# Optimization experiments

Measured on AMD Instinct MI355X. Metric: run time of the kernel, lower is better.

Reference implementation:

```python
import jax, jax.numpy as jnp
import numpy as np

B, C, H, W = 4, 256, 128, 128
HEADS = 64
HD = C // HEADS  # 4
G = 32           # group norm groups
EPS = 1e-5


def setup_inputs() -> dict:
    key = jax.random.key(0)
    ks = jax.random.split(key, 6)
    x = jax.random.normal(ks[0], (B, C, H, W), dtype=jnp.float32)
    gn_weight = jnp.ones((1, C, 1, 1), dtype=jnp.float32)
    gn_bias = jnp.zeros((1, C, 1, 1), dtype=jnp.float32)
    # 1x1 convs stored as (out_ch, in_ch) matrices
    qkv_w = jax.random.normal(ks[1], (3 * C, C), dtype=jnp.float32) * 0.02
    qkv_b = jax.random.normal(ks[2], (3 * C,), dtype=jnp.float32) * 0.01
    out_w = jax.random.normal(ks[3], (C, C), dtype=jnp.float32) * 0.02
    out_b = jax.random.normal(ks[4], (C,), dtype=jnp.float32) * 0.01
    return {"x": x, "gn_weight": gn_weight, "gn_bias": gn_bias,
            "qkv_w": qkv_w, "qkv_b": qkv_b, "out_w": out_w, "out_b": out_b}


def group_norm(x, weight, bias):
    n, c, h, w = x.shape
    xg = x.reshape(n, G, -1)
    mean = xg.mean(axis=-1, keepdims=True)
    var = jnp.var(xg, axis=-1, keepdims=True, ddof=1)  # torch.var default is unbiased
    xg = (xg - mean) / jnp.sqrt(var + EPS)
    return xg.reshape(n, c, h, w) * weight + bias


def conv1x1(x, w, b):
    # x: (B, Cin, H, W), w: (Cout, Cin)
    return jnp.einsum('bchw,oc->bohw', x, w) + b[None, :, None, None]


def reference(x, gn_weight, gn_bias, qkv_w, qkv_b, out_w, out_b):
    skip = x
    h = group_norm(x, gn_weight, gn_bias)
    qkv = conv1x1(h, qkv_w, qkv_b)                      # (B, 3C, H, W)
    qkv = qkv.reshape(B, HEADS, 3 * HD, H * W)
    q, k, v = jnp.split(qkv, 3, axis=2)                  # each (B, heads, hd, HW)
    scores = jnp.einsum('bhdn,bhen->bhde', q, k) / (HD ** 0.5)  # (B, heads, hd, hd)
    scores = jax.nn.softmax(scores, axis=1)              # softmax over HEADS axis (as in source)
    out = jnp.einsum('bhde,bhen->bhdn', scores, v)       # (B, heads, hd, HW)
    out = out.reshape(B, C, H, W)
    out = conv1x1(out, out_w, out_b)
    return out + skip
```

## Files before the change

kernel.cpp:

```cpp
#include <hip/hip_runtime.h>


constexpr int kB = 4;
constexpr int kC = 256;
constexpr int kHW = 16384;
constexpr int kHeads = 64;
constexpr int kNG = 32;
constexpr int kCPG = 8;
constexpr int kCP1 = 257;
constexpr int kPS = 260;
constexpr float kEPS = 1e-5f;
constexpr int kNSplit = 32;

typedef __attribute__((ext_vector_type(8))) _Float16 f16x8;
typedef __attribute__((ext_vector_type(4))) _Float16 f16x4;
typedef __attribute__((ext_vector_type(4))) float f32x4;

union V8 { f16x8 v; uint4 u; _Float16 h[8]; };

__device__ __forceinline__ void gload16(const void* g, void* l) {
  __builtin_amdgcn_global_load_lds(
      (const __attribute__((address_space(1))) void*)g,
      (__attribute__((address_space(3))) void*)l, 16, 0, 0);
}

constexpr size_t oXT    = 0;
constexpr size_t oXH    = oXT + (size_t)kB * kHW * kC / 2;
constexpr size_t oSpart = oXH + (size_t)kB * kHW * kC / 2;
constexpr size_t oS     = oSpart + (size_t)3 * kB * kNSplit * 128 * 128;
constexpr size_t oSums  = oS + (size_t)kB * kCP1 * kPS;
constexpr size_t oGv    = oSums + (size_t)kB * kC;
constexpr size_t oSc    = oGv + (size_t)kB * kC;
constexpr size_t oTc    = oSc + (size_t)kB * kC;
constexpr size_t oScore = oTc + (size_t)kB * kC;
constexpr size_t oAq    = oSpart;
constexpr size_t oM     = oXH;
constexpr size_t oGmH   = oXH + (size_t)kB * kC * kPS;

__global__ __launch_bounds__(256) void k0_tr(const float* __restrict__ x,
                                             _Float16* __restrict__ xT,
                                             _Float16* __restrict__ xH,
                                             float* __restrict__ sums) {
  const int nt = blockIdx.x, ct = blockIdx.y, b = blockIdx.z;
  __shared__ float T[64][65];
  __shared__ float psum[64][4];
  const float* xb = x + ((size_t)b * kC + ct * 64) * kHW + nt * 64;
  _Float16* xhb = xH + ((size_t)b * kC + ct * 64) * kHW + nt * 64;
  const int tid = threadIdx.x;

#pragma unroll
  for (int rep = 0; rep < 4; ++rep) {
    const int r = rep * 16 + (tid >> 4);
    const int c4 = (tid & 15) * 4;
    float4 v = *(const float4*)(xb + (size_t)r * kHW + c4);
    T[r][c4 + 0] = v.x; T[r][c4 + 1] = v.y; T[r][c4 + 2] = v.z; T[r][c4 + 3] = v.w;
    f16x4 hv = {(_Float16)v.x, (_Float16)v.y, (_Float16)v.z, (_Float16)v.w};
    *(f16x4*)(xhb + (size_t)r * kHW + c4) = hv;
  }
  __syncthreads();
  {
    const int q = tid >> 6, r = tid & 63;
    float s = 0.f;
#pragma unroll
    for (int i = 0; i < 16; ++i) s += T[r][q * 16 + i];
    psum[r][q] = s;
  }
  __syncthreads();
  if (tid < 64) {
    float s = psum[tid][0] + psum[tid][1] + psum[tid][2] + psum[tid][3];
    atomicAdd(&sums[b * kC + ct * 64 + tid], s);
  }
  const int nl = tid >> 2, cgrp = tid & 3;
  V8 lo, hi;
#pragma unroll
  for (int i = 0; i < 8; ++i)  lo.h[i] = (_Float16)T[cgrp * 16 + i][nl];
#pragma unroll
  for (int i = 0; i < 8; ++i)  hi.h[i] = (_Float16)T[cgrp * 16 + 8 + i][nl];
  _Float16* dst = xT + ((size_t)b * kHW + nt * 64 + nl) * kC + ct * 64 + cgrp * 16;
  *(uint4*)dst = lo.u;
  *(uint4*)(dst + 8) = hi.u;
}

__global__ __launch_bounds__(256) void k1_syrk(const _Float16* __restrict__ xH,
                                               float* __restrict__ Spart) {
  const int tt = blockIdx.x >> 5;
  const int sp = blockIdx.x & 31;
  const int b = blockIdx.y;
  const int ti = (tt == 2) ? 1 : 0;
  const int tj = (tt == 0) ? 0 : 1;
  const bool diag = (ti == tj);
  const _Float16* xb = xH + (size_t)b * kC * kHW;
  const int n0 = sp * (kHW / kNSplit);

  __shared__ __align__(16) _Float16 XI[2][128 * 64];
  __shared__ __align__(16) _Float16 XJ[2][128 * 64];

  const int tid = threadIdx.x;
  const int wave = tid >> 6, lane = tid & 63;
  const int wi = wave >> 1, wj = wave & 1;
  const int lrow = lane & 15, lgq = lane >> 4;
  const int srow = lane >> 3, sslot = lane & 7;

  const _Float16* srcI = xb + (size_t)(ti * 128) * kHW + n0;
  const _Float16* srcJ = xb + (size_t)(tj * 128) * kHW + n0;

  f32x4 acc[16];
#pragma unroll
  for (int i = 0; i < 16; ++i) acc[i] = (f32x4){0.f, 0.f, 0.f, 0.f};

  auto stage = [&](int buf, int nb) {
#pragma unroll
    for (int rep = 0; rep < 4; ++rep) {
      const int rr = rep * 32 + wave * 8 + srow;
      const int g = sslot ^ (rr & 7);
      char* dI = (char*)XI[buf] + (rep * 32 + wave * 8) * 128;
      gload16(srcI + (size_t)rr * kHW + nb + g * 8, dI);
      if (!diag) {
        char* dJ = (char*)XJ[buf] + (rep * 32 + wave * 8) * 128;
        gload16(srcJ + (size_t)rr * kHW + nb + g * 8, dJ);
      }
    }
  };

  stage(0, 0);
  __syncthreads();

  constexpr int NCH = kHW / kNSplit / 64;
  for (int ch = 0; ch < NCH; ++ch) {
    const int buf = ch & 1;
    if (ch + 1 < NCH) stage(buf ^ 1, (ch + 1) * 64);
    const _Float16* XIb = XI[buf];
    const _Float16* XBb = diag ? XI[buf] : XJ[buf];
#pragma unroll
    for (int sub = 0; sub < 2; ++sub) {
      const int gq = sub * 4 + lgq;
      f16x8 afr[4], bfr[4];
#pragma unroll
      for (int ia = 0; ia < 4; ++ia) {
        const int r = wi * 64 + ia * 16 + lrow;
        afr[ia] = *(const f16x8*)((const char*)XIb + (size_t)r * 128 + (((unsigned)(gq ^ (r & 7))) << 4));
      }
#pragma unroll
      for (int jb = 0; jb < 4; ++jb) {
        const int r = wj * 64 + jb * 16 + lrow;
        bfr[jb] = *(const f16x8*)((const char*)XBb + (size_t)r * 128 + (((unsigned)(gq ^ (r & 7))) << 4));
      }
#pragma unroll
      for (int ia = 0; ia < 4; ++ia)
#pragma unroll
        for (int jb = 0; jb < 4; ++jb)
          acc[ia * 4 + jb] = __builtin_amdgcn_mfma_f32_16x16x32_f16(afr[ia], bfr[jb], acc[ia * 4 + jb], 0, 0, 0);
    }
    __syncthreads();
  }
  float* P = Spart + (((size_t)tt * kB + b) * kNSplit + sp) * 16384;
#pragma unroll
  for (int ia = 0; ia < 4; ++ia)
#pragma unroll
    for (int jb = 0; jb < 4; ++jb)
#pragma unroll
      for (int reg = 0; reg < 4; ++reg) {
        const int i = wi * 64 + ia * 16 + lgq * 4 + reg;
        const int j = wj * 64 + jb * 16 + lrow;
        P[(size_t)i * 128 + j] = acc[ia * 4 + jb][reg];
      }
}

__global__ __launch_bounds__(256) void k1r_reduce(const float* __restrict__ Spart,
                                                  float* __restrict__ S) {
  const int blk = blockIdx.x;
  const int tile12 = blk >> 4;
  const int part = blk & 15;
  const int tt = tile12 >> 2, b = tile12 & 3;
  const int rti = (tt == 2) ? 1 : 0;
  const int rtj = (tt == 0) ? 0 : 1;
  const int e0 = part * 1024 + threadIdx.x * 4;
  float4 s = {0.f, 0.f, 0.f, 0.f};
  const float* base = Spart + ((size_t)tt * kB + b) * kNSplit * 16384 + e0;
  for (int sp = 0; sp < kNSplit; ++sp) {
    float4 v = *(const float4*)(base + (size_t)sp * 16384);
    s.x += v.x; s.y += v.y; s.z += v.z; s.w += v.w;
  }
  const int i = e0 >> 7, j = e0 & 127;
  float* Sb = S + (size_t)b * kCP1 * kPS;
  float* dst = Sb + (size_t)(rti * 128 + i) * kPS + rtj * 128 + j;
  dst[0] = s.x; dst[1] = s.y; dst[2] = s.z; dst[3] = s.w;
  if (tt == 1) {
    Sb[(size_t)(128 + j + 0) * kPS + i] = s.x;
    Sb[(size_t)(128 + j + 1) * kPS + i] = s.y;
    Sb[(size_t)(128 + j + 2) * kPS + i] = s.z;
    Sb[(size_t)(128 + j + 3) * kPS + i] = s.w;
  }
}

__global__ __launch_bounds__(256) void k2a_stats(const float* __restrict__ S,
                                                 const float* __restrict__ sums,
                                                 const float* __restrict__ gw,
                                                 const float* __restrict__ gb,
                                                 float* __restrict__ sArr,
                                                 float* __restrict__ tArr) {
  const int b = blockIdx.x;
  const float* Sb = S + (size_t)b * kCP1 * kPS;
  __shared__ float sx[kC], sdg[kC], meanv[kNG], invv[kNG];
  const int c = threadIdx.x;
  sx[c]  = sums[b * kC + c];
  sdg[c] = Sb[(size_t)c * kPS + c];
  __syncthreads();
  if (c < kNG) {
    float sum = 0.f, ssq = 0.f;
    for (int k = 0; k < kCPG; ++k) { sum += sx[c * kCPG + k]; ssq += sdg[c * kCPG + k]; }
    const float n = (float)(kCPG * kHW);
    const float mean = sum / n;
    const float var = (ssq - n * mean * mean) / (n - 1.0f);
    meanv[c] = mean;
    invv[c] = rsqrtf(var + kEPS);
  }
  __syncthreads();
  const int g = c / kCPG;
  const float s = gw[c] * invv[g];
  sArr[b * kC + c] = s;
  tArr[b * kC + c] = gb[c] - meanv[g] * s;
}

__global__ __launch_bounds__(256) void k3a_aq(const float* __restrict__ S,
                                              const float* __restrict__ sums,
                                              const float* __restrict__ sArr,
                                              const float* __restrict__ tArr,
                                              const float* __restrict__ qkv_w,
                                              const float* __restrict__ qkv_b,
                                              float* __restrict__ Aq) {
  const int ct = blockIdx.x, mt = blockIdx.y, b = blockIdx.z;
  const float* Sb = S + (size_t)b * kCP1 * kPS;
  const float HWf = (float)kHW;
  __shared__ float Wt[32][68];
  __shared__ float Gs[32][68];
  __shared__ float shs[kC], sht[kC], shx[kC], shr[kC];
  const int tid = threadIdx.x;
  {
    const float sv = sArr[b * kC + tid];
    const float tv = tArr[b * kC + tid];
    const float xv = sums[b * kC + tid];
    shs[tid] = sv; sht[tid] = tv; shx[tid] = xv;
    shr[tid] = sv * xv + tv * HWf;
  }
  __syncthreads();
  float acc[16];
#pragma unroll
  for (int i = 0; i < 16; ++i) acc[i] = 0.f;
  const int i0 = (tid & 15) * 4;
  const int j0 = (tid >> 4) * 4;
  const int cp0 = ct * 64;

  for (int cb = 0; cb < kC; cb += 32) {
    int idx = tid;
#pragma unroll
    for (int r = 0; r < 2; ++r) {
      const int m = idx >> 3;
      const int c4 = (idx & 7) * 4;
      const int mg = mt * 64 + m;
      const int row = 12 * (mg >> 2) + (mg & 3);
      float4 v = *(const float4*)(qkv_w + (size_t)row * kC + cb + c4);
      Wt[c4 + 0][m] = v.x; Wt[c4 + 1][m] = v.y; Wt[c4 + 2][m] = v.z; Wt[c4 + 3][m] = v.w;
      idx += 256;
    }
    idx = tid;
#pragma unroll
    for (int r = 0; r < 2; ++r) {
      const int cc = idx >> 4;
      const int n4 = (idx & 15) * 4;
      const int rr = cb + cc;
      const float s_r = shs[rr], t_r = sht[rr], x_r = shx[rr];
      float4 o;
      if (cp0 + n4 < kC) {
        float4 v = *(const float4*)(Sb + (size_t)rr * kPS + cp0 + n4);
        const int cp = cp0 + n4;
        o.x = s_r * (shs[cp + 0] * v.x + sht[cp + 0] * x_r) + t_r * shr[cp + 0];
        o.y = s_r * (shs[cp + 1] * v.y + sht[cp + 1] * x_r) + t_r * shr[cp + 1];
        o.z = s_r * (shs[cp + 2] * v.z + sht[cp + 2] * x_r) + t_r * shr[cp + 2];
        o.w = s_r * (shs[cp + 3] * v.w + sht[cp + 3] * x_r) + t_r * shr[cp + 3];
      } else if (cp0 + n4 == kC) {
        o = (float4){s_r * x_r + t_r * HWf, 0.f, 0.f, 0.f};
      } else {
        o = (float4){0.f, 0.f, 0.f, 0.f};
      }
      *(float4*)&Gs[cc][n4] = o;
      idx += 256;
    }
    __syncthreads();
#pragma unroll
    for (int kk = 0; kk < 32; ++kk) {
      float4 a = *(const float4*)&Wt[kk][i0];
      float4 g = *(const float4*)&Gs[kk][j0];
      acc[0]  += a.x * g.x; acc[1]  += a.x * g.y; acc[2]  += a.x * g.z; acc[3]  += a.x * g.w;
      acc[4]  += a.y * g.x; acc[5]  += a.y * g.y; acc[6]  += a.y * g.z; acc[7]  += a.y * g.w;
      acc[8]  += a.z * g.x; acc[9]  += a.z * g.y; acc[10] += a.z * g.z; acc[11] += a.z * g.w;
      acc[12] += a.w * g.x; acc[13] += a.w * g.y; acc[14] += a.w * g.z; acc[15] += a.w * g.w;
    }
    __syncthreads();
  }
#pragma unroll
  for (int mi = 0; mi < 4; ++mi) {
    const int mg = mt * 64 + i0 + mi;
    const float bias = qkv_b[12 * (mg >> 2) + (mg & 3)];
#pragma unroll
    for (int cj = 0; cj < 4; ++cj) {
      const int cp = cp0 + j0 + cj;
      if (cp < kCP1) {
        const float g256 = (cp < kC) ? shr[cp] : HWf;
        Aq[((size_t)b * kC + mg) * kCP1 + cp] = acc[mi * 4 + cj] + bias * g256;
      }
    }
  }
}

__global__ __launch_bounds__(256) void k3b_scores(const float* __restrict__ Aq,
                                                  const float* __restrict__ qkv_w,
                                                  const float* __restrict__ qkv_b,
                                                  float* __restrict__ score) {
  const int h = blockIdx.x, b = blockIdx.y;
  const int tid = threadIdx.x, wave = tid >> 6, lane = tid & 63;
#pragma unroll
  for (int p = wave; p < 16; p += 4) {
    const int d = p >> 2, e = p & 3;
    const float* aqr = Aq + ((size_t)b * kC + h * 4 + d) * kCP1;
    const int krow = h * 12 + 4 + e;
    float s = 0.f;
#pragma unroll
    for (int it = 0; it < 4; ++it) {
      const int cp = lane + it * 64;
      s += aqr[cp] * qkv_w[(size_t)krow * kC + cp];
    }
    if (lane == 0) s += aqr[256] * qkv_b[krow];
#pragma unroll
    for (int off = 32; off; off >>= 1) s += __shfl_xor(s, off);
    if (lane == 0) score[((size_t)(b * kHeads) + h) * 16 + p] = 0.5f * s;
  }
}

__global__ __launch_bounds__(256) void k45_M(const float* __restrict__ score,
                                             const float* __restrict__ qkv_w,
                                             const float* __restrict__ qkv_b,
                                             float* __restrict__ M) {
  const int b = blockIdx.y;
  const int cidx = blockIdx.x;
  const int h = cidx >> 2, d = cidx & 3;
  __shared__ float sc[64][4];
  __shared__ float mx[4], sm[4];
  const int tid = threadIdx.x;
  {
    const int h2 = tid >> 2, e = tid & 3;
    sc[h2][e] = score[((size_t)(b * kHeads) + h2) * 16 + d * 4 + e];
  }
  __syncthreads();
  const int wave = tid >> 6, lane = tid & 63;
  {
    const float v = sc[lane][wave];
    float m = v;
#pragma unroll
    for (int off = 32; off; off >>= 1) m = fmaxf(m, __shfl_xor(m, off));
    float e2 = expf(v - m);
#pragma unroll
    for (int off = 32; off; off >>= 1) e2 += __shfl_xor(e2, off);
    if (lane == 0) { mx[wave] = m; sm[wave] = e2; }
  }
  __syncthreads();
  const float p0 = expf(sc[h][0] - mx[0]) / sm[0];
  const float p1 = expf(sc[h][1] - mx[1]) / sm[1];
  const float p2 = expf(sc[h][2] - mx[2]) / sm[2];
  const float p3 = expf(sc[h][3] - mx[3]) / sm[3];
  for (int cp = tid; cp < kCP1; cp += 256) {
    float a;
    if (cp < kC) {
      a = p0 * qkv_w[(size_t)(h * 12 + 8 + 0) * kC + cp] +
          p1 * qkv_w[(size_t)(h * 12 + 8 + 1) * kC + cp] +
          p2 * qkv_w[(size_t)(h * 12 + 8 + 2) * kC + cp] +
          p3 * qkv_w[(size_t)(h * 12 + 8 + 3) * kC + cp];
    } else {
      a = p0 * qkv_b[h * 12 + 8 + 0] + p1 * qkv_b[h * 12 + 8 + 1] +
          p2 * qkv_b[h * 12 + 8 + 2] + p3 * qkv_b[h * 12 + 8 + 3];
    }
    M[((size_t)b * kC + cidx) * kPS + cp] = a;
  }
}

__global__ __launch_bounds__(256) void k5b_gemm(const float* __restrict__ M,
                                                const float* __restrict__ out_w,
                                                const float* __restrict__ sArr,
                                                const float* __restrict__ tArr,
                                                _Float16* __restrict__ GmH,
                                                float* __restrict__ gvec) {
  const int ct = blockIdx.x, ot = blockIdx.y, b = blockIdx.z;
  const float* Mb = M + (size_t)b * kC * kPS;
  __shared__ float Wt[32][68];
  __shared__ float Gs[32][68];
  __shared__ float gred[64][17];
  float acc[16];
#pragma unroll
  for (int i = 0; i < 16; ++i) acc[i] = 0.f;
  const int tid = threadIdx.x;
  const int i0 = (tid & 15) * 4;
  const int j0 = (tid >> 4) * 4;
  const int cp0 = ct * 64;

  for (int cb = 0; cb < kC; cb += 32) {
    int idx = tid;
#pragma unroll
    for (int r = 0; r < 2; ++r) {
      const int m = idx >> 3;
      const int c4 = (idx & 7) * 4;
      float4 v = *(const float4*)(out_w + (size_t)(ot * 64 + m) * kC + cb + c4);
      Wt[c4 + 0][m] = v.x; Wt[c4 + 1][m] = v.y; Wt[c4 + 2][m] = v.z; Wt[c4 + 3][m] = v.w;
      idx += 256;
    }
    idx = tid;
#pragma unroll
    for (int r = 0; r < 2; ++r) {
      const int cc = idx >> 4;
      const int n4 = (idx & 15) * 4;
      float4 v = {0.f, 0.f, 0.f, 0.f};
      if (cp0 + n4 < kCP1) v = *(const float4*)(Mb + (size_t)(cb + cc) * kPS + cp0 + n4);
      *(float4*)&Gs[cc][n4] = v;
      idx += 256;
    }
    __syncthreads();
#pragma unroll
    for (int kk = 0; kk < 32; ++kk) {
      float4 a = *(const float4*)&Wt[kk][i0];
      float4 g = *(const float4*)&Gs[kk][j0];
      acc[0]  += a.x * g.x; acc[1]  += a.x * g.y; acc[2]  += a.x * g.z; acc[3]  += a.x * g.w;
      acc[4]  += a.y * g.x; acc[5]  += a.y * g.y; acc[6]  += a.y * g.z; acc[7]  += a.y * g.w;
      acc[8]  += a.z * g.x; acc[9]  += a.z * g.y; acc[10] += a.z * g.z; acc[11] += a.z * g.w;
      acc[12] += a.w * g.x; acc[13] += a.w * g.y; acc[14] += a.w * g.z; acc[15] += a.w * g.w;
    }
    __syncthreads();
  }
  float gpart[4] = {0.f, 0.f, 0.f, 0.f};
#pragma unroll
  for (int mi = 0; mi < 4; ++mi) {
    const int o = ot * 64 + i0 + mi;
#pragma unroll
    for (int cj = 0; cj < 4; ++cj) {
      const int cp = cp0 + j0 + cj;
      const float f = acc[mi * 4 + cj];
      if (cp < kC) {
        GmH[((size_t)b * kC + o) * kC + cp] = (_Float16)(f * sArr[b * kC + cp]);
        gpart[mi] += f * tArr[b * kC + cp];
      } else if (cp == kC) {
        gpart[mi] += f;
      }
    }
  }
#pragma unroll
  for (int mi = 0; mi < 4; ++mi) gred[i0 + mi][tid >> 4] = gpart[mi];
  __syncthreads();
  if (tid < 64) {
    float s = 0.f;
#pragma unroll
    for (int k = 0; k < 16; ++k) s += gred[tid][k];
    atomicAdd(&gvec[b * kC + ot * 64 + tid], s);
  }
}

__global__ __launch_bounds__(256) void k6_final(const _Float16* __restrict__ xT,
                                                const _Float16* __restrict__ GmH,
                                                const float* __restrict__ gvec,
                                                const float* __restrict__ out_b,
                                                const float* __restrict__ x,
                                                float* __restrict__ out) {
  const int nt = blockIdx.x, ot = blockIdx.y, b = blockIdx.z;
  __shared__ __align__(16) char smem[64 * 132 * 4];
  float* Ep = (float*)smem;
  const int tid = threadIdx.x;
  const int wave = tid >> 6, lane = tid & 63;
  const int wo = wave >> 1, wn = wave & 1;
  const int lrow = lane & 15, lgq = lane >> 4;
  const int srow = lane >> 3, sslot = lane & 7;

  const _Float16* xrow = xT + ((size_t)b * kHW + nt * 128) * kC;
  const _Float16* Grow = GmH + (size_t)(b * kC + ot * 128) * kC;

  auto stage = [&](int buf, int cc) {
#pragma unroll
    for (int rep = 0; rep < 4; ++rep) {
      const int rr = rep * 32 + wave * 8 + srow;
      const int g = sslot ^ (rr & 7);
      gload16(xrow + (size_t)rr * kC + cc + g * 8,
              smem + buf * 16384 + (rep * 32 + wave * 8) * 128);
    }
  };

  f32x4 acc[16];
#pragma unroll
  for (int i = 0; i < 16; ++i) acc[i] = (f32x4){0.f, 0.f, 0.f, 0.f};

  stage(0, 0);
  __syncthreads();

  for (int ci = 0; ci < 4; ++ci) {
    const int cc = ci * 64;
    const int buf = ci & 1;
    if (ci < 3) stage(buf ^ 1, cc + 64);
    const char* XB = smem + buf * 16384;
#pragma unroll
    for (int sub = 0; sub < 2; ++sub) {
      const int gq = sub * 4 + lgq;
      f16x8 afr[4], bfr[4];
#pragma unroll
      for (int ia = 0; ia < 4; ++ia) {
        const int r = wo * 64 + ia * 16 + lrow;
        afr[ia] = *(const f16x8*)(Grow + (size_t)r * kC + cc + gq * 8);
      }
#pragma unroll
      for (int jb = 0; jb < 4; ++jb) {
        const int r = wn * 64 + jb * 16 + lrow;
        bfr[jb] = *(const f16x8*)(XB + (size_t)r * 128 + (((unsigned)(gq ^ (r & 7))) << 4));
      }
#pragma unroll
      for (int ia = 0; ia < 4; ++ia)
#pragma unroll
        for (int jb = 0; jb < 4; ++jb)
          acc[ia * 4 + jb] = __builtin_amdgcn_mfma_f32_16x16x32_f16(afr[ia], bfr[jb], acc[ia * 4 + jb], 0, 0, 0);
    }
    __syncthreads();
  }
#pragma unroll
  for (int p = 0; p < 2; ++p) {
    if (wo == p) {
#pragma unroll
      for (int ia = 0; ia < 4; ++ia)
#pragma unroll
        for (int jb = 0; jb < 4; ++jb)
#pragma unroll
          for (int reg = 0; reg < 4; ++reg)
            Ep[(size_t)(ia * 16 + lgq * 4 + reg) * 132 + wn * 64 + jb * 16 + lrow] =
                acc[ia * 4 + jb][reg];
    }
    __syncthreads();
#pragma unroll
    for (int it = 0; it < 8; ++it) {
      const int id = it * 256 + tid;
      const int row = id >> 5, nc = (id & 31) * 4;
      const int o = ot * 128 + p * 64 + row;
      const float gvv = gvec[b * kC + o] + out_b[o];
      float4 e = *(const float4*)&Ep[(size_t)row * 132 + nc];
      const size_t gidx = ((size_t)b * kC + o) * kHW + nt * 128 + nc;
      float4 sk = *(const float4*)&x[gidx];
      float4 res = {e.x + gvv + sk.x, e.y + gvv + sk.y, e.z + gvv + sk.z, e.w + gvv + sk.w};
      *(float4*)&out[gidx] = res;
    }
    __syncthreads();
  }
}

extern "C" void kernel_launch(void* const* d_in, const int* in_sizes, int n_in,
                              void* d_out, int out_size, void* d_ws, size_t ws_size,
                              hipStream_t stream) {
  const float* x    = (const float*)d_in[0];
  const float* gnw  = (const float*)d_in[1];
  const float* gnb  = (const float*)d_in[2];
  const float* qkvw = (const float*)d_in[3];
  const float* qkvb = (const float*)d_in[4];
  const float* outw = (const float*)d_in[5];
  const float* outb = (const float*)d_in[6];
  float* out = (float*)d_out;
  float* ws = (float*)d_ws;

  _Float16* xT   = (_Float16*)(ws + oXT);
  _Float16* xH   = (_Float16*)(ws + oXH);
  float* Spart   = ws + oSpart;
  float* S       = ws + oS;
  float* sums    = ws + oSums;
  float* gv      = ws + oGv;
  float* sArr    = ws + oSc;
  float* tArr    = ws + oTc;
  float* score   = ws + oScore;
  float* Aq      = ws + oAq;
  float* M       = ws + oM;
  _Float16* GmH  = (_Float16*)(ws + oGmH);

  hipMemsetAsync(sums, 0, (size_t)2 * kB * kC * sizeof(float), stream);
  k0_tr<<<dim3(kHW / 64, kC / 64, kB), 256, 0, stream>>>(x, xT, xH, sums);
  k1_syrk<<<dim3(3 * kNSplit, kB), 256, 0, stream>>>(xH, Spart);
  k1r_reduce<<<dim3(3 * kB * 16), 256, 0, stream>>>(Spart, S);
  k2a_stats<<<kB, 256, 0, stream>>>(S, sums, gnw, gnb, sArr, tArr);
  k3a_aq<<<dim3(5, 4, kB), 256, 0, stream>>>(S, sums, sArr, tArr, qkvw, qkvb, Aq);
  k3b_scores<<<dim3(kHeads, kB), 256, 0, stream>>>(Aq, qkvw, qkvb, score);
  k45_M<<<dim3(kC, kB), 256, 0, stream>>>(score, qkvw, qkvb, M);
  k5b_gemm<<<dim3(5, 4, kB), 256, 0, stream>>>(M, outw, sArr, tArr, GmH, gv);
  k6_final<<<dim3(kHW / 128, kC / 128, kB), 256, 0, stream>>>(xT, GmH, gv, outb, x, out);
}
```

Measured before the change: 243.4 us.

## Fuse group-norm stats into consumers, shuffle-reduce sums, widen reduce grid

Removes the separate k2a_stats kernel. The group-norm mean and inverse std are now recomputed redundantly inside k3a_aq and k5b_gemm from S and sums. k0_tr now loads 8 floats per thread and computes row sums with a wave shuffle, issuing one atomic per row segment instead of doing a shared-memory reduction with an extra barrier. k1r_reduce doubles its block count with float2 loads and an unrolled loop to raise parallelism. The trade-off is one fewer launch and sync point against redundant per-block stats work and more atomics in k0.

```diff
diff --git a/kernel.cpp b/kernel.cpp
--- a/kernel.cpp
+++ b/kernel.cpp
@@ -30,9 +30,7 @@
 constexpr size_t oS     = oSpart + (size_t)3 * kB * kNSplit * 128 * 128;
 constexpr size_t oSums  = oS + (size_t)kB * kCP1 * kPS;
 constexpr size_t oGv    = oSums + (size_t)kB * kC;
-constexpr size_t oSc    = oGv + (size_t)kB * kC;
-constexpr size_t oTc    = oSc + (size_t)kB * kC;
-constexpr size_t oScore = oTc + (size_t)kB * kC;
+constexpr size_t oScore = oGv + (size_t)kB * kC;
 constexpr size_t oAq    = oSpart;
 constexpr size_t oM     = oXH;
 constexpr size_t oGmH   = oXH + (size_t)kB * kC * kPS;
@@ -43,33 +41,32 @@
                                              float* __restrict__ sums) {
   const int nt = blockIdx.x, ct = blockIdx.y, b = blockIdx.z;
   __shared__ float T[64][65];
-  __shared__ float psum[64][4];
   const float* xb = x + ((size_t)b * kC + ct * 64) * kHW + nt * 64;
   _Float16* xhb = xH + ((size_t)b * kC + ct * 64) * kHW + nt * 64;
   const int tid = threadIdx.x;
-
-#pragma unroll
-  for (int rep = 0; rep < 4; ++rep) {
-    const int r = rep * 16 + (tid >> 4);
-    const int c4 = (tid & 15) * 4;
-    float4 v = *(const float4*)(xb + (size_t)r * kHW + c4);
-    T[r][c4 + 0] = v.x; T[r][c4 + 1] = v.y; T[r][c4 + 2] = v.z; T[r][c4 + 3] = v.w;
-    f16x4 hv = {(_Float16)v.x, (_Float16)v.y, (_Float16)v.z, (_Float16)v.w};
-    *(f16x4*)(xhb + (size_t)r * kHW + c4) = hv;
-  }
-  __syncthreads();
-  {
-    const int q = tid >> 6, r = tid & 63;
-    float s = 0.f;
-#pragma unroll
-    for (int i = 0; i < 16; ++i) s += T[r][q * 16 + i];
-    psum[r][q] = s;
-  }
-  __syncthreads();
-  if (tid < 64) {
-    float s = psum[tid][0] + psum[tid][1] + psum[tid][2] + psum[tid][3];
-    atomicAdd(&sums[b * kC + ct * 64 + tid], s);
-  }
+  const int lane = tid & 63;
+
+#pragma unroll
+  for (int rep = 0; rep < 2; ++rep) {
+    const int r = rep * 32 + (tid >> 3);
+    const int c8 = (tid & 7) * 8;
+    float4 v0 = *(const float4*)(xb + (size_t)r * kHW + c8);
+    float4 v1 = *(const float4*)(xb + (size_t)r * kHW + c8 + 4);
+    T[r][c8 + 0] = v0.x; T[r][c8 + 1] = v0.y; T[r][c8 + 2] = v0.z; T[r][c8 + 3] = v0.w;
+    T[r][c8 + 4] = v1.x; T[r][c8 + 5] = v1.y; T[r][c8 + 6] = v1.z; T[r][c8 + 7] = v1.w;
+    V8 h;
+    h.h[0] = (_Float16)v0.x; h.h[1] = (_Float16)v0.y;
+    h.h[2] = (_Float16)v0.z; h.h[3] = (_Float16)v0.w;
+    h.h[4] = (_Float16)v1.x; h.h[5] = (_Float16)v1.y;
+    h.h[6] = (_Float16)v1.z; h.h[7] = (_Float16)v1.w;
+    *(uint4*)(xhb + (size_t)r * kHW + c8) = h.u;
+    float rs = v0.x + v0.y + v0.z + v0.w + v1.x + v1.y + v1.z + v1.w;
+    rs += __shfl_xor(rs, 1);
+    rs += __shfl_xor(rs, 2);
+    rs += __shfl_xor(rs, 4);
+    if ((lane & 7) == 0) atomicAdd(&sums[b * kC + ct * 64 + r], rs);
+  }
+  __syncthreads();
   const int nl = tid >> 2, cgrp = tid & 3;
   V8 lo, hi;
 #pragma unroll
@@ -169,63 +166,33 @@
 __global__ __launch_bounds__(256) void k1r_reduce(const float* __restrict__ Spart,
                                                   float* __restrict__ S) {
   const int blk = blockIdx.x;
-  const int tile12 = blk >> 4;
-  const int part = blk & 15;
+  const int tile12 = blk >> 5;
+  const int part = blk & 31;
   const int tt = tile12 >> 2, b = tile12 & 3;
   const int rti = (tt == 2) ? 1 : 0;
   const int rtj = (tt == 0) ? 0 : 1;
-  const int e0 = part * 1024 + threadIdx.x * 4;
-  float4 s = {0.f, 0.f, 0.f, 0.f};
+  const int e0 = part * 512 + threadIdx.x * 2;
+  float2 s = {0.f, 0.f};
   const float* base = Spart + ((size_t)tt * kB + b) * kNSplit * 16384 + e0;
+#pragma unroll 8
   for (int sp = 0; sp < kNSplit; ++sp) {
-    float4 v = *(const float4*)(base + (size_t)sp * 16384);
-    s.x += v.x; s.y += v.y; s.z += v.z; s.w += v.w;
+    float2 v = *(const float2*)(base + (size_t)sp * 16384);
+    s.x += v.x; s.y += v.y;
   }
   const int i = e0 >> 7, j = e0 & 127;
   float* Sb = S + (size_t)b * kCP1 * kPS;
   float* dst = Sb + (size_t)(rti * 128 + i) * kPS + rtj * 128 + j;
-  dst[0] = s.x; dst[1] = s.y; dst[2] = s.z; dst[3] = s.w;
+  dst[0] = s.x; dst[1] = s.y;
   if (tt == 1) {
     Sb[(size_t)(128 + j + 0) * kPS + i] = s.x;
     Sb[(size_t)(128 + j + 1) * kPS + i] = s.y;
-    Sb[(size_t)(128 + j + 2) * kPS + i] = s.z;
-    Sb[(size_t)(128 + j + 3) * kPS + i] = s.w;
-  }
-}
-
-__global__ __launch_bounds__(256) void k2a_stats(const float* __restrict__ S,
-                                                 const float* __restrict__ sums,
-                                                 const float* __restrict__ gw,
-                                                 const float* __restrict__ gb,
-                                                 float* __restrict__ sArr,
-                                                 float* __restrict__ tArr) {
-  const int b = blockIdx.x;
-  const float* Sb = S + (size_t)b * kCP1 * kPS;
-  __shared__ float sx[kC], sdg[kC], meanv[kNG], invv[kNG];
-  const int c = threadIdx.x;
-  sx[c]  = sums[b * kC + c];
-  sdg[c] = Sb[(size_t)c * kPS + c];
-  __syncthreads();
-  if (c < kNG) {
-    float sum = 0.f, ssq = 0.f;
-    for (int k = 0; k < kCPG; ++k) { sum += sx[c * kCPG + k]; ssq += sdg[c * kCPG + k]; }
-    const float n = (float)(kCPG * kHW);
-    const float mean = sum / n;
-    const float var = (ssq - n * mean * mean) / (n - 1.0f);
-    meanv[c] = mean;
-    invv[c] = rsqrtf(var + kEPS);
-  }
-  __syncthreads();
-  const int g = c / kCPG;
-  const float s = gw[c] * invv[g];
-  sArr[b * kC + c] = s;
-  tArr[b * kC + c] = gb[c] - meanv[g] * s;
+  }
 }
 
 __global__ __launch_bounds__(256) void k3a_aq(const float* __restrict__ S,
                                               const float* __restrict__ sums,
-                                              const float* __restrict__ sArr,
-                                              const float* __restrict__ tArr,
+                                              const float* __restrict__ gw,
+                                              const float* __restrict__ gb,
                                               const float* __restrict__ qkv_w,
                                               const float* __restrict__ qkv_b,
                                               float* __restrict__ Aq) {
@@ -235,13 +202,27 @@
   __shared__ float Wt[32][68];
   __shared__ float Gs[32][68];
   __shared__ float shs[kC], sht[kC], shx[kC], shr[kC];
+  __shared__ float meanv[kNG], invv[kNG];
   const int tid = threadIdx.x;
+  shx[tid] = sums[b * kC + tid];
+  sht[tid] = Sb[(size_t)tid * kPS + tid];
+  __syncthreads();
+  if (tid < kNG) {
+    float sum = 0.f, ssq = 0.f;
+#pragma unroll
+    for (int k = 0; k < kCPG; ++k) { sum += shx[tid * kCPG + k]; ssq += sht[tid * kCPG + k]; }
+    const float n = (float)(kCPG * kHW);
+    const float mean = sum / n;
+    const float var = (ssq - n * mean * mean) / (n - 1.0f);
+    meanv[tid] = mean;
+    invv[tid] = rsqrtf(var + kEPS);
+  }
+  __syncthreads();
   {
-    const float sv = sArr[b * kC + tid];
-    const float tv = tArr[b * kC + tid];
-    const float xv = sums[b * kC + tid];
-    shs[tid] = sv; sht[tid] = tv; shx[tid] = xv;
-    shr[tid] = sv * xv + tv * HWf;
+    const float sv = gw[tid] * invv[tid / kCPG];
+    const float tv = gb[tid] - meanv[tid / kCPG] * sv;
+    shs[tid] = sv; sht[tid] = tv;
+    shr[tid] = sv * shx[tid] + tv * HWf;
   }
   __syncthreads();
   float acc[16];
@@ -385,19 +366,46 @@
 
 __global__ __launch_bounds__(256) void k5b_gemm(const float* __restrict__ M,
                                                 const float* __restrict__ out_w,
-                                                const float* __restrict__ sArr,
-                                                const float* __restrict__ tArr,
+                                                const float* __restrict__ S,
+                                                const float* __restrict__ sums,
+                                                const float* __restrict__ gw,
+                                                const float* __restrict__ gb,
                                                 _Float16* __restrict__ GmH,
                                                 float* __restrict__ gvec) {
   const int ct = blockIdx.x, ot = blockIdx.y, b = blockIdx.z;
   const float* Mb = M + (size_t)b * kC * kPS;
+  const float* Sb = S + (size_t)b * kCP1 * kPS;
   __shared__ float Wt[32][68];
   __shared__ float Gs[32][68];
   __shared__ float gred[64][17];
+  __shared__ float sS[kC], sT[kC];
+  __shared__ float meanv[kNG], invv[kNG];
+  const int tid = threadIdx.x;
+  sS[tid] = sums[b * kC + tid];
+  sT[tid] = Sb[(size_t)tid * kPS + tid];
+  __syncthreads();
+  if (tid < kNG) {
+    float sum = 0.f, ssq = 0.f;
+#pragma unroll
+    for (int k = 0; k < kCPG; ++k) { sum += sS[tid * kCPG + k]; ssq += sT[tid * kCPG + k]; }
+    const float n = (float)(kCPG * kHW);
+    const float mean = sum / n;
+    const float var = (ssq - n * mean * mean) / (n - 1.0f);
+    meanv[tid] = mean;
+    invv[tid] = rsqrtf(var + kEPS);
+  }
+  __syncthreads();
+  {
+    const float xv = sS[tid];
+    const float sv = gw[tid] * invv[tid / kCPG];
+    sS[tid] = sv;
+    sT[tid] = gb[tid] - meanv[tid / kCPG] * sv;
+    (void)xv;
+  }
+  __syncthreads();
   float acc[16];
 #pragma unroll
   for (int i = 0; i < 16; ++i) acc[i] = 0.f;
-  const int tid = threadIdx.x;
   const int i0 = (tid & 15) * 4;
   const int j0 = (tid >> 4) * 4;
   const int cp0 = ct * 64;
@@ -443,8 +451,8 @@
       const int cp = cp0 + j0 + cj;
       const float f = acc[mi * 4 + cj];
       if (cp < kC) {
-        GmH[((size_t)b * kC + o) * kC + cp] = (_Float16)(f * sArr[b * kC + cp]);
-        gpart[mi] += f * tArr[b * kC + cp];
+        GmH[((size_t)b * kC + o) * kC + cp] = (_Float16)(f * sS[cp]);
+        gpart[mi] += f * sT[cp];
       } else if (cp == kC) {
         gpart[mi] += f;
       }
@@ -571,8 +579,6 @@
   float* S       = ws + oS;
   float* sums    = ws + oSums;
   float* gv      = ws + oGv;
-  float* sArr    = ws + oSc;
-  float* tArr    = ws + oTc;
   float* score   = ws + oScore;
   float* Aq      = ws + oAq;
   float* M       = ws + oM;
@@ -581,11 +587,10 @@
   hipMemsetAsync(sums, 0, (size_t)2 * kB * kC * sizeof(float), stream);
   k0_tr<<<dim3(kHW / 64, kC / 64, kB), 256, 0, stream>>>(x, xT, xH, sums);
   k1_syrk<<<dim3(3 * kNSplit, kB), 256, 0, stream>>>(xH, Spart);
-  k1r_reduce<<<dim3(3 * kB * 16), 256, 0, stream>>>(Spart, S);
-  k2a_stats<<<kB, 256, 0, stream>>>(S, sums, gnw, gnb, sArr, tArr);
-  k3a_aq<<<dim3(5, 4, kB), 256, 0, stream>>>(S, sums, sArr, tArr, qkvw, qkvb, Aq);
+  k1r_reduce<<<dim3(3 * kB * 32), 256, 0, stream>>>(Spart, S);
+  k3a_aq<<<dim3(5, 4, kB), 256, 0, stream>>>(S, sums, gnw, gnb, qkvw, qkvb, Aq);
   k3b_scores<<<dim3(kHeads, kB), 256, 0, stream>>>(Aq, qkvw, qkvb, score);
   k45_M<<<dim3(kC, kB), 256, 0, stream>>>(score, qkvw, qkvb, M);
-  k5b_gemm<<<dim3(5, 4, kB), 256, 0, stream>>>(M, outw, sArr, tArr, GmH, gv);
+  k5b_gemm<<<dim3(5, 4, kB), 256, 0, stream>>>(M, outw, S, sums, gnw, gnb, GmH, gv);
   k6_final<<<dim3(kHW / 128, kC / 128, kB), 256, 0, stream>>>(xT, GmH, gv, outb, x, out);
 }
```

Result: no change. 247.0 us (+1.5%).
